# Performance work log

Hardware: AMD Instinct MI355X
Metric: run time of the kernel (lower is better)

The kernel has to match this reference:

```python
import jax, jax.numpy as jnp
import numpy as np

B, L, D, H = 8, 1024, 512, 8
EPS = 1e-5

def setup_inputs() -> dict:
    key = jax.random.key(0)
    ks = jax.random.split(key, 12)
    s = lambda fan_in: 1.0 / np.sqrt(fan_in)
    u = lambda k, shape, sc: jax.random.uniform(k, shape, jnp.float32, -sc, sc)
    return {
        "input": jax.random.normal(ks[0], (B, L, D), jnp.float32),
        "wq": u(ks[1], (D, H * D), s(D)), "bq": u(ks[2], (H * D,), s(D)),
        "wk": u(ks[3], (D, H * D), s(D)), "bk": u(ks[4], (H * D,), s(D)),
        "wv": u(ks[5], (D, H * D), s(D)), "bv": u(ks[6], (H * D,), s(D)),
        "score_w": u(ks[7], (2 * D, 1), s(2 * D)), "score_b": u(ks[8], (1,), s(2 * D)),
        "fc_w": u(ks[9], (H * D, D), s(H * D)), "fc_b": u(ks[10], (D,), s(H * D)),
        "ln_g": jnp.ones((D,), jnp.float32), "ln_b": jnp.zeros((D,), jnp.float32),
    }

def reference(input, wq, bq, wk, bk, wv, bv, score_w, score_b, fc_w, fc_b, ln_g, ln_b):
    x = input
    b, l, d = x.shape
    h = wq.shape[1] // d
    # project and fold heads into leading batch dim: (h*b, l, d)
    def proj(w, bias):
        y = (x @ w + bias).reshape(b, l, h, d)
        return y.transpose(2, 0, 1, 3).reshape(h * b, l, d)
    q = proj(wq, bq)
    k = proj(wk, bk)
    v = proj(wv, bv)
    # _score(cat(k_i, q_j)) decomposed: k part uses score_w[:d], q part score_w[d:]
    sk = (k @ score_w[:d])[:, :, 0]   # (h*b, l) -> row index i
    sq = (q @ score_w[d:])[:, :, 0]   # (h*b, l) -> col index j
    kq = jnp.tanh(sk[:, :, None] + sq[:, None, :] + score_b[0])  # (h*b, l, l)
    # faithful to original bug: softmax over trailing size-1 dim -> all ones
    score = jax.nn.softmax(kq[..., None], axis=-1)[..., 0]       # (h*b, l, l)
    out = jnp.einsum('nij,njd->nid', score, v)                   # (h*b, l, d)
    out = out.reshape(h, b, l, d).transpose(1, 2, 0, 3).reshape(b, l, h * d)
    out = out @ fc_w + fc_b
    y = out + x
    mu = jnp.mean(y, axis=-1, keepdims=True)
    var = jnp.var(y, axis=-1, keepdims=True)
    return (y - mu) / jnp.sqrt(var + EPS) * ln_g + ln_b
```

## Files before the change

kernel.cpp:

```cpp
#include <hip/hip_runtime.h>

#define BB 8
#define LL 1024
#define DD 512
#define HDIM 4096
#define EPS_LN 1e-5f
#define NB 256
#define NT 1024
#define POISON_I ((int)0xAAAAAAAAu)


__device__ __forceinline__ void grid_bar(int* base, int g, int my) {
    asm volatile("s_waitcnt vmcnt(0)" ::: "memory");
    __syncthreads();
    if (threadIdx.x == 0) {
        int v = __hip_atomic_fetch_add(base + (1 + g) * 32, 1,
                                       __ATOMIC_RELAXED,
                                       __HIP_MEMORY_SCOPE_AGENT);
        bool released = false;
        if (v == POISON_I + 31) {
            int m = __hip_atomic_fetch_add(base, 1, __ATOMIC_RELAXED,
                                           __HIP_MEMORY_SCOPE_AGENT);
            if (m == POISON_I + 7) {
                __builtin_amdgcn_fence(__ATOMIC_RELEASE, "agent");
#pragma unroll
                for (int r = 0; r < 8; ++r)
                    __hip_atomic_store(base + (9 + r) * 32, 1,
                                       __ATOMIC_RELAXED,
                                       __HIP_MEMORY_SCOPE_AGENT);
                released = true;
            }
        }
        if (!released) {
            int* f = base + (9 + my) * 32;
            while (__hip_atomic_load(f, __ATOMIC_RELAXED,
                                     __HIP_MEMORY_SCOPE_AGENT) != 1)
                __builtin_amdgcn_s_sleep(1);
        }
        asm volatile("" ::: "memory");
    }
    __syncthreads();
}

__global__ __launch_bounds__(NT) void mha_fused(
    const float* __restrict__ x,
    const float* __restrict__ wv,
    const float* __restrict__ bv,
    const float* __restrict__ fcw,
    const float* __restrict__ fcb,
    const float* __restrict__ g,
    const float* __restrict__ beta,
    float* __restrict__ out,
    float* __restrict__ xs,
    float* __restrict__ u,
    int* __restrict__ bar)
{
    __shared__ float redA[16][DD];
    __shared__ float xs_lds[BB * DD];
    __shared__ float Tpart[64][144];
    __shared__ float Tpart2[8][144];
    __shared__ float T_lds[BB * 16];
    __shared__ float uf[DD];

    const int tid = threadIdx.x;
    const int bi  = blockIdx.x;
    const int b   = bi >> 5;
    const int gB  = bi >> 5;
    const int my  = bi & 7;

    const int dv   = tid & 63;
    const int rowg = tid >> 6;
    float4 xa0, xa1, xb0, xb1;

    {
        const float* basep = x + ((size_t)(bi * 32 + rowg * 2)) * DD + dv * 8;
        xa0 = *(const float4*)(basep);
        xa1 = *(const float4*)(basep + 4);
        xb0 = *(const float4*)(basep + DD);
        xb1 = *(const float4*)(basep + DD + 4);

        float4* dst = (float4*)&redA[rowg][dv * 8];
        dst[0] = make_float4(xa0.x + xb0.x, xa0.y + xb0.y,
                             xa0.z + xb0.z, xa0.w + xb0.w);
        dst[1] = make_float4(xa1.x + xb1.x, xa1.y + xb1.y,
                             xa1.z + xb1.z, xa1.w + xb1.w);
        __syncthreads();

        if (tid < DD) {
            float s = 0.f;
#pragma unroll
            for (int gg = 0; gg < 16; ++gg) s += redA[gg][tid];
            atomicAdd(&xs[b * DD + tid], s);
        }
    }

    const int chunk = ((bi & 7) << 5) | (bi >> 3);
    const int c0  = chunk * 16;
    const int cB  = tid & 15;
    const int kg  = tid >> 4;
    const int ddB = tid & 511;
    const int bh  = tid >> 9;

    float wvp[8];
#pragma unroll
    for (int j = 0; j < 8; ++j)
        wvp[j] = wv[(size_t)(kg * 8 + j) * HDIM + c0 + cB];
    float fcp[16];
#pragma unroll
    for (int cc = 0; cc < 16; ++cc)
        fcp[cc] = fcw[(size_t)(c0 + cc) * DD + ddB];

    grid_bar(bar, gB, my);

    {
        ((float4*)xs_lds)[tid] = ((const float4*)xs)[tid];
        __syncthreads();

        float acc[BB];
#pragma unroll
        for (int bb = 0; bb < BB; ++bb) acc[bb] = 0.f;
#pragma unroll
        for (int j = 0; j < 8; ++j) {
            const int k = kg * 8 + j;
#pragma unroll
            for (int bb = 0; bb < BB; ++bb)
                acc[bb] += xs_lds[bb * DD + k] * wvp[j];
        }
#pragma unroll
        for (int bb = 0; bb < BB; ++bb) Tpart[kg][bb * 16 + cB] = acc[bb];
        __syncthreads();

        {
            const int e   = tid & 127;
            const int sub = tid >> 7;
            float s = 0.f;
#pragma unroll
            for (int q = 0; q < 8; ++q) s += Tpart[sub * 8 + q][e];
            Tpart2[sub][e] = s;
        }
        __syncthreads();
        if (tid < BB * 16) {
            float s = 0.f;
#pragma unroll
            for (int q = 0; q < 8; ++q) s += Tpart2[q][tid];
            s += 1024.f * bv[c0 + (tid & 15)];
            T_lds[tid] = s;
        }
        __syncthreads();

        float accu[4] = {0.f, 0.f, 0.f, 0.f};
#pragma unroll
        for (int cc = 0; cc < 16; ++cc) {
            float f = fcp[cc];
#pragma unroll
            for (int q = 0; q < 4; ++q)
                accu[q] += T_lds[(bh * 4 + q) * 16 + cc] * f;
        }
#pragma unroll
        for (int q = 0; q < 4; ++q)
            atomicAdd(&u[(bh * 4 + q) * DD + ddB], accu[q]);
    }

    grid_bar(bar + 1024, gB, my);

    {
        if (tid < DD) uf[tid] = u[b * DD + tid] + fcb[tid];
        __syncthreads();

        const int lane = dv;
        float4 uq0 = *(const float4*)(uf + lane * 8);
        float4 uq1 = *(const float4*)(uf + lane * 8 + 4);
        float4 g0 = *(const float4*)(g + lane * 8);
        float4 g1 = *(const float4*)(g + lane * 8 + 4);
        float4 b0 = *(const float4*)(beta + lane * 8);
        float4 b1 = *(const float4*)(beta + lane * 8 + 4);

#pragma unroll
        for (int it = 0; it < 2; ++it) {
            const int row = bi * 32 + rowg * 2 + it;
            const size_t off = (size_t)row * DD + lane * 8;
            float4 x0 = (it == 0) ? xa0 : xb0;
            float4 x1 = (it == 0) ? xa1 : xb1;

            float y[8];
            y[0] = x0.x + uq0.x;  y[1] = x0.y + uq0.y;
            y[2] = x0.z + uq0.z;  y[3] = x0.w + uq0.w;
            y[4] = x1.x + uq1.x;  y[5] = x1.y + uq1.y;
            y[6] = x1.z + uq1.z;  y[7] = x1.w + uq1.w;

            float s1 = 0.f, ss = 0.f;
#pragma unroll
            for (int i = 0; i < 8; ++i) { s1 += y[i]; ss += y[i] * y[i]; }
#pragma unroll
            for (int m = 1; m < 64; m <<= 1) {
                s1 += __shfl_xor(s1, m, 64);
                ss += __shfl_xor(ss, m, 64);
            }
            const float mean = s1 * (1.f / 512.f);
            const float var  = ss * (1.f / 512.f) - mean * mean;
            const float rstd = rsqrtf(var + EPS_LN);

            float4 o0, o1;
            o0.x = (y[0] - mean) * rstd * g0.x + b0.x;
            o0.y = (y[1] - mean) * rstd * g0.y + b0.y;
            o0.z = (y[2] - mean) * rstd * g0.z + b0.z;
            o0.w = (y[3] - mean) * rstd * g0.w + b0.w;
            o1.x = (y[4] - mean) * rstd * g1.x + b1.x;
            o1.y = (y[5] - mean) * rstd * g1.y + b1.y;
            o1.z = (y[6] - mean) * rstd * g1.z + b1.z;
            o1.w = (y[7] - mean) * rstd * g1.w + b1.w;
            *(float4*)(out + off)     = o0;
            *(float4*)(out + off + 4) = o1;
        }
    }
}

extern "C" void kernel_launch(void* const* d_in, const int* in_sizes, int n_in,
                              void* d_out, int out_size, void* d_ws, size_t ws_size,
                              hipStream_t stream) {
    const float* x   = (const float*)d_in[0];
    const float* wv  = (const float*)d_in[5];
    const float* bv  = (const float*)d_in[6];
    const float* fcw = (const float*)d_in[9];
    const float* fcb = (const float*)d_in[10];
    const float* lng = (const float*)d_in[11];
    const float* lnb = (const float*)d_in[12];

    float* xs  = (float*)d_ws;
    int*   bar = (int*)((char*)d_ws + 16 * 1024);
    float* u   = (float*)((char*)d_ws + 32 * 1024);
    float* out = (float*)d_out;

    mha_fused<<<NB, NT, 0, stream>>>(x, wv, bv, fcw, fcb, lng, lnb,
                                     out, xs, u, bar);
}
```

Measured before the change: 121.5 us.

## Replace grid-wide barriers with per-batch barriers and per-batch weight partitioning

```diff
diff --git a/kernel.cpp b/kernel.cpp
--- a/kernel.cpp
+++ b/kernel.cpp
@@ -10,33 +10,16 @@
 #define POISON_I ((int)0xAAAAAAAAu)
 
 
-__device__ __forceinline__ void grid_bar(int* base, int g, int my) {
+__device__ __forceinline__ void batch_bar(int* cnt) {
     asm volatile("s_waitcnt vmcnt(0)" ::: "memory");
     __syncthreads();
     if (threadIdx.x == 0) {
-        int v = __hip_atomic_fetch_add(base + (1 + g) * 32, 1,
-                                       __ATOMIC_RELAXED,
-                                       __HIP_MEMORY_SCOPE_AGENT);
-        bool released = false;
-        if (v == POISON_I + 31) {
-            int m = __hip_atomic_fetch_add(base, 1, __ATOMIC_RELAXED,
-                                           __HIP_MEMORY_SCOPE_AGENT);
-            if (m == POISON_I + 7) {
-                __builtin_amdgcn_fence(__ATOMIC_RELEASE, "agent");
-#pragma unroll
-                for (int r = 0; r < 8; ++r)
-                    __hip_atomic_store(base + (9 + r) * 32, 1,
-                                       __ATOMIC_RELAXED,
-                                       __HIP_MEMORY_SCOPE_AGENT);
-                released = true;
-            }
-        }
-        if (!released) {
-            int* f = base + (9 + my) * 32;
-            while (__hip_atomic_load(f, __ATOMIC_RELAXED,
-                                     __HIP_MEMORY_SCOPE_AGENT) != 1)
-                __builtin_amdgcn_s_sleep(1);
-        }
+        __hip_atomic_fetch_add(cnt, 1, __ATOMIC_RELAXED,
+                               __HIP_MEMORY_SCOPE_AGENT);
+        while (__hip_atomic_load(cnt, __ATOMIC_RELAXED,
+                                 __HIP_MEMORY_SCOPE_AGENT) !=
+               POISON_I + 32)
+            __builtin_amdgcn_s_sleep(1);
         asm volatile("" ::: "memory");
     }
     __syncthreads();
@@ -56,17 +39,15 @@
     int* __restrict__ bar)
 {
     __shared__ float redA[16][DD];
-    __shared__ float xs_lds[BB * DD];
-    __shared__ float Tpart[64][144];
-    __shared__ float Tpart2[8][144];
-    __shared__ float T_lds[BB * 16];
+    __shared__ float xs_b[DD];
+    __shared__ float Tpart[8][128];
+    __shared__ float T_l[128];
     __shared__ float uf[DD];
 
     const int tid = threadIdx.x;
     const int bi  = blockIdx.x;
     const int b   = bi >> 5;
-    const int gB  = bi >> 5;
-    const int my  = bi & 7;
+    const int j   = bi & 31;
 
     const int dv   = tid & 63;
     const int rowg = tid >> 6;
@@ -94,74 +75,45 @@
         }
     }
 
-    const int chunk = ((bi & 7) << 5) | (bi >> 3);
-    const int c0  = chunk * 16;
-    const int cB  = tid & 15;
-    const int kg  = tid >> 4;
-    const int ddB = tid & 511;
-    const int bh  = tid >> 9;
-
-    float wvp[8];
-#pragma unroll
-    for (int j = 0; j < 8; ++j)
-        wvp[j] = wv[(size_t)(kg * 8 + j) * HDIM + c0 + cB];
-    float fcp[16];
-#pragma unroll
-    for (int cc = 0; cc < 16; ++cc)
-        fcp[cc] = fcw[(size_t)(c0 + cc) * DD + ddB];
-
-    grid_bar(bar, gB, my);
+    batch_bar(bar + b * 32);
 
     {
-        ((float4*)xs_lds)[tid] = ((const float4*)xs)[tid];
+        const int c0 = j * 128;
+        if (tid < DD) xs_b[tid] = xs[b * DD + tid];
         __syncthreads();
 
-        float acc[BB];
-#pragma unroll
-        for (int bb = 0; bb < BB; ++bb) acc[bb] = 0.f;
-#pragma unroll
-        for (int j = 0; j < 8; ++j) {
-            const int k = kg * 8 + j;
-#pragma unroll
-            for (int bb = 0; bb < BB; ++bb)
-                acc[bb] += xs_lds[bb * DD + k] * wvp[j];
+        const int cI = tid & 127;
+        const int kg = tid >> 7;
+        float t = 0.f;
+        const float* wcol = wv + c0 + cI;
+#pragma unroll 8
+        for (int i = 0; i < 64; ++i) {
+            const int k = kg * 64 + i;
+            t += xs_b[k] * wcol[(size_t)k * HDIM];
         }
-#pragma unroll
-        for (int bb = 0; bb < BB; ++bb) Tpart[kg][bb * 16 + cB] = acc[bb];
+        Tpart[kg][cI] = t;
         __syncthreads();
 
-        {
-            const int e   = tid & 127;
-            const int sub = tid >> 7;
+        if (tid < 128) {
             float s = 0.f;
 #pragma unroll
-            for (int q = 0; q < 8; ++q) s += Tpart[sub * 8 + q][e];
-            Tpart2[sub][e] = s;
-        }
-        __syncthreads();
-        if (tid < BB * 16) {
-            float s = 0.f;
-#pragma unroll
-            for (int q = 0; q < 8; ++q) s += Tpart2[q][tid];
-            s += 1024.f * bv[c0 + (tid & 15)];
-            T_lds[tid] = s;
+            for (int q = 0; q < 8; ++q) s += Tpart[q][tid];
+            T_l[tid] = s + 1024.f * bv[c0 + tid];
         }
         __syncthreads();
 
-        float accu[4] = {0.f, 0.f, 0.f, 0.f};
-#pragma unroll
-        for (int cc = 0; cc < 16; ++cc) {
-            float f = fcp[cc];
-#pragma unroll
-            for (int q = 0; q < 4; ++q)
-                accu[q] += T_lds[(bh * 4 + q) * 16 + cc] * f;
+        const int dd = tid & 511;
+        const int ch = tid >> 9;
+        float a = 0.f;
+#pragma unroll 8
+        for (int i = 0; i < 64; ++i) {
+            const int c = ch * 64 + i;
+            a += T_l[c] * fcw[(size_t)(c0 + c) * DD + dd];
         }
-#pragma unroll
-        for (int q = 0; q < 4; ++q)
-            atomicAdd(&u[(bh * 4 + q) * DD + ddB], accu[q]);
+        atomicAdd(&u[b * DD + dd], a);
     }
 
-    grid_bar(bar + 1024, gB, my);
+    batch_bar(bar + (8 + b) * 32);
 
     {
         if (tid < DD) uf[tid] = u[b * DD + tid] + fcb[tid];
```

Result: faster. 117.6 us (-3.2%).
